# Kernel tuning notes

Measured on AMD Instinct MI355X. Metric: run time of the kernel, lower is better.

Reference implementation:

```python
import jax, jax.numpy as jnp
from jax import lax
import numpy as np

# db3 analysis/synthesis filter bank (pywt coefficients)
DEC_LO = np.array([0.035226291882100656, -0.085441273882241486, -0.13501102001039084,
                   0.45987750211933132, 0.80689150931333875, 0.33267055295095688], dtype=np.float32)
DEC_HI = np.array([-0.33267055295095688, 0.80689150931333875, -0.45987750211933132,
                   -0.13501102001039084, 0.085441273882241486, 0.035226291882100656], dtype=np.float32)
REC_LO = DEC_LO[::-1].copy()
REC_HI = np.array([0.035226291882100656, 0.085441273882241486, -0.13501102001039084,
                   -0.45987750211933132, 0.80689150931333875, -0.33267055295095688], dtype=np.float32)
L = 6  # db3 filter length
DN = ('NCHW', 'OIHW', 'NCHW')

# analysis correlation kernels (torch conv2d correlates, pytorch_wavelets pre-flips dec filters)
H0_A = jnp.asarray(DEC_LO[::-1].copy())
H1_A = jnp.asarray(DEC_HI[::-1].copy())
# synthesis: conv_transpose(x, g, stride=2, pad=L-2) == correlate(dilate(x,2), flip(g), pad=1)
G0_S = jnp.asarray(REC_LO[::-1].copy())
G1_S = jnp.asarray(REC_HI[::-1].copy())


def _sep_conv(x, f, axis, stride=1, lhs_dil=1, pad=0):
    """Depthwise 1-D correlation along H (axis=2) or W (axis=3) of an NCHW tensor."""
    C = x.shape[1]
    if axis == 2:
        k = jnp.tile(f.reshape(1, 1, -1, 1), (C, 1, 1, 1))
        strides, dil, padding = (stride, 1), (lhs_dil, 1), ((pad, pad), (0, 0))
    else:
        k = jnp.tile(f.reshape(1, 1, 1, -1), (C, 1, 1, 1))
        strides, dil, padding = (1, stride), (1, lhs_dil), ((0, 0), (pad, pad))
    return lax.conv_general_dilated(x, k, strides, padding, lhs_dilation=dil,
                                    dimension_numbers=DN, feature_group_count=C)


def _dwt2(x):
    # single-level separable 2D DWT, mode='zero' (pytorch_wavelets: rows then cols)
    lo = _sep_conv(x, H0_A, 3, stride=2, pad=L - 2)
    hi = _sep_conv(x, H1_A, 3, stride=2, pad=L - 2)
    ll = _sep_conv(lo, H0_A, 2, stride=2, pad=L - 2)
    lh = _sep_conv(lo, H1_A, 2, stride=2, pad=L - 2)  # yh[:,:,0]
    hl = _sep_conv(hi, H0_A, 2, stride=2, pad=L - 2)  # yh[:,:,1]
    hh = _sep_conv(hi, H1_A, 2, stride=2, pad=L - 2)  # yh[:,:,2]
    return ll, lh, hl, hh


def _idwt2(ll, lh, hl, hh):
    # inverse: cols then rows; transposed conv realized as lhs_dilation=2 + pad 1
    lo = _sep_conv(ll, G0_S, 2, lhs_dil=2, pad=1) + _sep_conv(lh, G1_S, 2, lhs_dil=2, pad=1)
    hi = _sep_conv(hl, G0_S, 2, lhs_dil=2, pad=1) + _sep_conv(hh, G1_S, 2, lhs_dil=2, pad=1)
    return _sep_conv(lo, G0_S, 3, lhs_dil=2, pad=1) + _sep_conv(hi, G1_S, 3, lhs_dil=2, pad=1)


def _dw3x3(x, w):
    # depthwise 3x3, padding 1, no bias; w: (C,1,3,3)
    return lax.conv_general_dilated(x, w, (1, 1), ((1, 1), (1, 1)),
                                    dimension_numbers=DN, feature_group_count=x.shape[1])


def _ssl(x, conv5_w, conv7_w, conv9_w):
    # faithful to original: conv5 applied to BOTH yl and ylh; conv1/conv_cat unused
    ll, lh, hl, hh = _dwt2(x)
    return _idwt2(_dw3x3(ll, conv5_w), _dw3x3(lh, conv5_w),
                  _dw3x3(hl, conv7_w), _dw3x3(hh, conv9_w))


def setup_inputs() -> dict:
    key = jax.random.key(0)
    ks = jax.random.split(key, 7)
    B, C, H, W, HEADS = 4, 256, 192, 192, 8
    s = 0.05
    return {
        'x': jax.random.normal(ks[0], (B, C, H, W), jnp.float32),
        'qkv_w': jax.random.normal(ks[1], (2 * C, C), jnp.float32) * s,        # 1x1 conv C->2C
        'qkv_conv_w': jax.random.normal(ks[2], (2 * C, 1, 3, 3), jnp.float32) * s,  # depthwise 3x3
        'conv5_w': jax.random.normal(ks[3], (C, 1, 3, 3), jnp.float32) * s,
        'conv7_w': jax.random.normal(ks[4], (C, 1, 3, 3), jnp.float32) * s,
        'conv9_w': jax.random.normal(ks[5], (C, 1, 3, 3), jnp.float32) * s,
        'proj_w': jax.random.normal(ks[6], (C, C), jnp.float32) * s,           # 1x1 conv C->C
        'temperature': jnp.ones((1, HEADS, 1, 1), jnp.float32),
        'num_heads': HEADS,
    }


def reference(x, qkv_w, qkv_conv_w, conv5_w, conv7_w, conv9_w, proj_w, temperature, num_heads):
    b, c, h, w = x.shape
    eps = 1e-12
    kv = jnp.einsum('oc,bchw->bohw', qkv_w, x)          # 1x1 conv, no bias
    kv = _dw3x3(kv, qkv_conv_w)
    k, v = jnp.split(kv, 2, axis=1)
    q = _ssl(x, conv5_w, conv7_w, conv9_w)              # wavelet query path, same HxW
    d = c // num_heads
    q = q.reshape(b, num_heads, d, h * w)
    k = k.reshape(b, num_heads, d, h * w)
    v = v.reshape(b, num_heads, d, h * w)
    q = q / jnp.maximum(jnp.linalg.norm(q, axis=-1, keepdims=True), eps)
    k = k / jnp.maximum(jnp.linalg.norm(k, axis=-1, keepdims=True), eps)
    attn = jax.nn.softmax(jnp.einsum('bhdn,bhen->bhde', q, k) * temperature, axis=-1)  # (b,H,d,d)
    out = jnp.einsum('bhde,bhen->bhdn', attn, v).reshape(b, c, h, w)
    return jnp.einsum('oc,bchw->bohw', proj_w, out)
```

## Files before the change

kernel.cpp:

```cpp
#include <hip/hip_runtime.h>
#include <hip/hip_bf16.h>

typedef __hip_bfloat16 bf16;
typedef __attribute__((ext_vector_type(8))) short short8v;
typedef __attribute__((ext_vector_type(4))) float f32x4;

#define NB 4
#define NC 256
#define NPIX 36864
#define NH 192
#define NW 192
#define SW 98
#define SH 98
#define GCH 24

__device__ __constant__ float cH0A[6] = {  0.33267055295095688f,  0.80689150931333875f,  0.45987750211933132f, -0.13501102001039084f, -0.085441273882241486f, 0.035226291882100656f };
__device__ __constant__ float cH1A[6] = {  0.035226291882100656f, 0.085441273882241486f, -0.13501102001039084f, -0.45987750211933132f,  0.80689150931333875f, -0.33267055295095688f };
__device__ __constant__ float cG0S[6] = {  0.035226291882100656f, -0.085441273882241486f, -0.13501102001039084f, 0.45987750211933132f,  0.80689150931333875f,  0.33267055295095688f };
__device__ __constant__ float cG1S[6] = { -0.33267055295095688f,  0.80689150931333875f, -0.45987750211933132f, -0.13501102001039084f,  0.085441273882241486f, 0.035226291882100656f };

__device__ inline unsigned short bfbits(float f) {
    bf16 h = __float2bfloat16(f);
    return *reinterpret_cast<unsigned short*>(&h);
}
__device__ inline float b2f(short s) {
    return __bfloat162float(*reinterpret_cast<const bf16*>(&s));
}

__global__ __launch_bounds__(256) void k_wave(const float* __restrict__ x,
                                              const float* __restrict__ w5, const float* __restrict__ w7,
                                              const float* __restrict__ w9,
                                              bf16* __restrict__ q, float* __restrict__ qsum) {
    int w0 = blockIdx.x * 64, h0 = blockIdx.y * 32;
    int bc = blockIdx.z;
    int c = bc & 255;
    int jh0 = h0 >> 1, jw0 = w0 >> 1;
    int xr0 = h0 - 6;
    int xc0 = w0 - 8;
    __shared__ __align__(16) char smem[40320];
    float (*s_x)[80]   = (float(*)[80])smem;
    float (*s_c)[36]   = (float(*)[36])smem;
    float (*s_lo)[40]  = (float(*)[40])(smem + 14080);
    float (*s_hi)[40]  = (float(*)[40])(smem + 21120);
    float (*s_lh)[36]  = (float(*)[36])(smem + 14080);
    float (*s_sub)[38] = (float(*)[38])(smem + 28160);
    __shared__ float s_w[4][9];
    __shared__ float red[4];
    const float* xp = x + (size_t)bc * NPIX;
    int t = threadIdx.x;
    if (t < 36) {
        int f = t / 9, k = t - f * 9;
        const float* wsel = (f <= 1) ? w5 : (f == 2 ? w7 : w9);
        s_w[f][k] = wsel[c * 9 + k];
    }
    for (int e = t; e < 880; e += 256) {
        int r = e / 20, s = e - r * 20;
        int row = xr0 + r, col0 = xc0 + s * 4;
        float4 v = make_float4(0.f, 0.f, 0.f, 0.f);
        if (row >= 0 && row < NH) {
            if (col0 >= 0 && col0 + 3 < NW) {
                v = *reinterpret_cast<const float4*>(xp + (size_t)row * NW + col0);
            } else {
#pragma unroll
                for (int j = 0; j < 4; ++j) {
                    int cc = col0 + j;
                    if (cc >= 0 && cc < NW) (&v.x)[j] = xp[(size_t)row * NW + cc];
                }
            }
        }
        *reinterpret_cast<float4*>(&s_x[r][s * 4]) = v;
    }
    __syncthreads();
    for (int e = t; e < 1672; e += 256) {
        int r = e / 38, jc = e - r * 38;
        float la = 0.f, ha = 0.f;
#pragma unroll
        for (int tp = 0; tp < 6; ++tp) {
            float v = s_x[r][2 * jc + tp];
            la = fmaf(v, cH0A[tp], la);
            ha = fmaf(v, cH1A[tp], ha);
        }
        s_lo[r][jc] = la; s_hi[r][jc] = ha;
    }
    __syncthreads();
    for (int e = t; e < 760; e += 256) {
        int r = e / 38, jc = e - r * 38;
        int gr = jh0 - 1 + r, gcol = jw0 - 2 + jc;
        bool inb = (gr >= 0 && gr < SH && gcol >= 0 && gcol < SW);
        float ll = 0.f, lh = 0.f, hl = 0.f, hh = 0.f;
#pragma unroll
        for (int tp = 0; tp < 6; ++tp) {
            float lv = s_lo[2 * r + tp][jc];
            float hv = s_hi[2 * r + tp][jc];
            ll = fmaf(lv, cH0A[tp], ll); lh = fmaf(lv, cH1A[tp], lh);
            hl = fmaf(hv, cH0A[tp], hl); hh = fmaf(hv, cH1A[tp], hh);
        }
        s_sub[r][jc]      = inb ? ll : 0.f;
        s_sub[20 + r][jc] = inb ? lh : 0.f;
        s_sub[40 + r][jc] = inb ? hl : 0.f;
        s_sub[60 + r][jc] = inb ? hh : 0.f;
    }
    __syncthreads();
    for (int e = t; e < 2448; e += 256) {
        int pr = e / 34, cc = e - pr * 34;
        int pl = pr / 18, r = pr - pl * 18;
        const float* wp = s_w[pl];
        const int rb = pl * 20 + r;
        float a = 0.f;
#pragma unroll
        for (int ky = 0; ky < 3; ++ky)
#pragma unroll
            for (int kx = 0; kx < 3; ++kx)
                a = fmaf(s_sub[rb + ky][cc + 1 + kx], wp[ky * 3 + kx], a);
        s_c[pr][cc] = a;
    }
    __syncthreads();
    for (int e = t; e < 1088; e += 256) {
        int row = e / 34, cc = e - row * 34;
        int which = row >> 4, m = row & 15;
        float c0_0 = s_c[which * 36 + m][cc],     c1_0 = s_c[which * 36 + 18 + m][cc];
        float c0_1 = s_c[which * 36 + m + 1][cc], c1_1 = s_c[which * 36 + 18 + m + 1][cc];
        float c0_2 = s_c[which * 36 + m + 2][cc], c1_2 = s_c[which * 36 + 18 + m + 2][cc];
        float ae = c0_0 * cG0S[1] + c0_1 * cG0S[3] + c0_2 * cG0S[5]
                 + c1_0 * cG1S[1] + c1_1 * cG1S[3] + c1_2 * cG1S[5];
        float ao = c0_0 * cG0S[0] + c0_1 * cG0S[2] + c0_2 * cG0S[4]
                 + c1_0 * cG1S[0] + c1_1 * cG1S[2] + c1_2 * cG1S[4];
        s_lh[which * 32 + 2 * m][cc] = ae;
        s_lh[which * 32 + 2 * m + 1][cc] = ao;
    }
    __syncthreads();
    float lsum = 0.f;
    bf16* qp = q + (size_t)bc * NPIX;
#pragma unroll
    for (int it = 0; it < 4; ++it) {
        int e = t + 256 * it;
        int hh = e >> 5, m = e & 31;
        float l0 = s_lh[hh][m],     h0v = s_lh[32 + hh][m];
        float l1 = s_lh[hh][m + 1], h1v = s_lh[32 + hh][m + 1];
        float l2 = s_lh[hh][m + 2], h2v = s_lh[32 + hh][m + 2];
        float ae = l0 * cG0S[1] + l1 * cG0S[3] + l2 * cG0S[5]
                 + h0v * cG1S[1] + h1v * cG1S[3] + h2v * cG1S[5];
        float ao = l0 * cG0S[0] + l1 * cG0S[2] + l2 * cG0S[4]
                 + h0v * cG1S[0] + h1v * cG1S[2] + h2v * cG1S[4];
        unsigned pack = (unsigned)bfbits(ae) | ((unsigned)bfbits(ao) << 16);
        *reinterpret_cast<unsigned*>(qp + (size_t)(h0 + hh) * NW + w0 + 2 * m) = pack;
        lsum = fmaf(ae, ae, lsum);
        lsum = fmaf(ao, ao, lsum);
    }
#pragma unroll
    for (int off = 32; off; off >>= 1) lsum += __shfl_down(lsum, off, 64);
    if ((t & 63) == 0) red[t >> 6] = lsum;
    __syncthreads();
    if (t == 0) atomicAdd(&qsum[bc], red[0] + red[1] + red[2] + red[3]);
}

__global__ __launch_bounds__(256) void k_xpose(const float* __restrict__ x, bf16* __restrict__ xT) {
    __shared__ float T[64][68];
    int nt = blockIdx.x, ct = blockIdx.y, b = blockIdx.z;
    int n0 = nt * 64, c0 = ct * 64;
    const float* xb = x + ((size_t)b * NC + c0) * NPIX + n0;
    int t = threadIdx.x;
    int tr = t >> 4, tc4 = (t & 15) * 4;
#pragma unroll
    for (int i = 0; i < 4; ++i) {
        int cc = tr + i * 16;
        float4 v = *reinterpret_cast<const float4*>(xb + (size_t)cc * NPIX + tc4);
        T[cc][tc4] = v.x; T[cc][tc4 + 1] = v.y; T[cc][tc4 + 2] = v.z; T[cc][tc4 + 3] = v.w;
    }
    __syncthreads();
    bf16* ob = xT + ((size_t)b * NPIX + n0) * NC + c0;
#pragma unroll
    for (int i = 0; i < 4; ++i) {
        int nn = tr + i * 16;
        ushort4 u;
        u.x = bfbits(T[tc4][nn]); u.y = bfbits(T[tc4 + 1][nn]);
        u.z = bfbits(T[tc4 + 2][nn]); u.w = bfbits(T[tc4 + 3][nn]);
        *reinterpret_cast<ushort4*>(ob + (size_t)nn * NC + tc4) = u;
    }
}

__global__ __launch_bounds__(256) void k_cvtw(const float* __restrict__ w, bf16* __restrict__ wb) {
    int idx = blockIdx.x * 256 + threadIdx.x;
    if (idx < 512 * 256) wb[idx] = __float2bfloat16(w[idx]);
}

template <typename TOUT>
__global__ __launch_bounds__(256) void k_gemm_bf(const bf16* __restrict__ X, const bf16* __restrict__ Wm,
                                                 int wStride, TOUT* __restrict__ Out) {
    __shared__ __align__(16) short As[128 * 64];
    __shared__ __align__(16) short Bs[128 * 64];
    int nt = blockIdx.x, ot = blockIdx.y, b = blockIdx.z;
    int n0 = nt * 128, o0 = ot * 128;
    const bf16* xb = X + (size_t)b * NPIX * NC;
    const bf16* Wb = Wm + (size_t)b * wStride;
    int t = threadIdx.x;
    int wv = t >> 6, l = t & 63;
    int wr = wv >> 1, wc = wv & 1;
    int lrow = l >> 3, cbs0 = l & 7;
    f32x4 z4 = {0.f, 0.f, 0.f, 0.f};
    f32x4 acc[4][4];
#pragma unroll
    for (int m = 0; m < 4; ++m)
#pragma unroll
        for (int nf = 0; nf < 4; ++nf) acc[m][nf] = z4;
    for (int kc = 0; kc < 256; kc += 64) {
        __syncthreads();
#pragma unroll
        for (int i = 0; i < 4; ++i) {
            int r0 = wv * 32 + i * 8;
            int r = r0 + lrow;
            int cb = cbs0 ^ (r & 7);
            __builtin_amdgcn_global_load_lds(
                (const __attribute__((address_space(1))) void*)(Wb + (size_t)(o0 + r) * NC + kc + cb * 8),
                (__attribute__((address_space(3))) void*)(As + r0 * 64), 16, 0, 0);
            __builtin_amdgcn_global_load_lds(
                (const __attribute__((address_space(1))) void*)(xb + (size_t)(n0 + r) * NC + kc + cb * 8),
                (__attribute__((address_space(3))) void*)(Bs + r0 * 64), 16, 0, 0);
        }
        __syncthreads();
#pragma unroll
        for (int kk = 0; kk < 2; ++kk) {
            int col8 = kk * 4 + (l >> 4);
            short8v av[4], bv[4];
#pragma unroll
            for (int m = 0; m < 4; ++m) {
                int row = wr * 64 + m * 16 + (l & 15);
                av[m] = *(const short8v*)(As + row * 64 + (col8 ^ (row & 7)) * 8);
            }
#pragma unroll
            for (int nf = 0; nf < 4; ++nf) {
                int row = wc * 64 + nf * 16 + (l & 15);
                bv[nf] = *(const short8v*)(Bs + row * 64 + (col8 ^ (row & 7)) * 8);
            }
#pragma unroll
            for (int m = 0; m < 4; ++m)
#pragma unroll
                for (int nf = 0; nf < 4; ++nf)
                    acc[m][nf] = __builtin_amdgcn_mfma_f32_16x16x32_bf16(av[m], bv[nf], acc[m][nf], 0, 0, 0);
        }
    }
    TOUT* ob = Out + (size_t)b * NC * NPIX;
#pragma unroll
    for (int m = 0; m < 4; ++m)
#pragma unroll
        for (int nf = 0; nf < 4; ++nf)
#pragma unroll
            for (int r = 0; r < 4; ++r) {
                int oo = o0 + wr * 64 + m * 16 + (l >> 4) * 4 + r;
                int nn = n0 + wc * 64 + nf * 16 + (l & 15);
                if constexpr (sizeof(TOUT) == 2)
                    ob[(size_t)oo * NPIX + nn] = __float2bfloat16(acc[m][nf][r]);
                else
                    ob[(size_t)oo * NPIX + nn] = acc[m][nf][r];
            }
}

__device__ inline short8v dw8(const bf16* __restrict__ chan, int r, int cb,
                              const float* __restrict__ w, float& ks) {
    float v[3][10];
#pragma unroll
    for (int ri = 0; ri < 3; ++ri) {
        int r2 = r + ri - 1;
        if (r2 < 0 || r2 >= NH) {
#pragma unroll
            for (int j = 0; j < 10; ++j) v[ri][j] = 0.f;
        } else {
            const bf16* p = chan + (size_t)r2 * NW + cb;
            short8v m = *(const short8v*)p;
            v[ri][0] = (cb > 0) ? __bfloat162float(p[-1]) : 0.f;
#pragma unroll
            for (int j = 0; j < 8; ++j) v[ri][j + 1] = b2f(m[j]);
            v[ri][9] = (cb < 184) ? __bfloat162float(p[8]) : 0.f;
        }
    }
    short8v out;
#pragma unroll
    for (int j = 0; j < 8; ++j) {
        float a = 0.f;
#pragma unroll
        for (int ri = 0; ri < 3; ++ri) {
            a = fmaf(v[ri][j],     w[ri * 3 + 0], a);
            a = fmaf(v[ri][j + 1], w[ri * 3 + 1], a);
            a = fmaf(v[ri][j + 2], w[ri * 3 + 2], a);
        }
        ks = fmaf(a, a, ks);
        out[j] = (short)bfbits(a);
    }
    return out;
}

__global__ __launch_bounds__(256) void k_gram_dw(const bf16* __restrict__ qbf, const bf16* __restrict__ kraw,
                                                 const float* __restrict__ dwW,
                                                 float* __restrict__ gpart, float* __restrict__ ksum) {
    int chunk = blockIdx.x;
    int bh = blockIdx.y; int b = bh >> 3, h = bh & 7;
    const bf16* qb = qbf + ((size_t)b * NC + h * 32) * NPIX;
    const bf16* kb = kraw + ((size_t)b * NC + h * 32) * NPIX;
    __shared__ float sg[4][1024];
    __shared__ float ksh[32];
    int t = threadIdx.x;
    int wv = t >> 6, l = t & 63;
    int dlo = l & 15, kslot = l >> 4;
    float wA[9], wB[9];
#pragma unroll
    for (int i = 0; i < 9; ++i) {
        wA[i] = dwW[(h * 32 + dlo) * 9 + i];
        wB[i] = dwW[(h * 32 + dlo + 16) * 9 + i];
    }
    const bf16* q0 = qb + (size_t)dlo * NPIX;
    const bf16* q1 = qb + (size_t)(dlo + 16) * NPIX;
    const bf16* k0 = kb + (size_t)dlo * NPIX;
    const bf16* k1 = kb + (size_t)(dlo + 16) * NPIX;
    f32x4 z4 = {0.f, 0.f, 0.f, 0.f};
    f32x4 a00 = z4, a01 = z4, a10 = z4, a11 = z4;
    float ks0 = 0.f, ks1 = 0.f;
    int r0 = chunk * 8 + wv * 2;
#pragma unroll
    for (int rr = 0; rr < 2; ++rr) {
        int r = r0 + rr;
#pragma unroll
        for (int c0 = 0; c0 < 192; c0 += 32) {
            int cb = c0 + kslot * 8;
            short8v av0 = *(const short8v*)(q0 + (size_t)r * NW + cb);
            short8v av1 = *(const short8v*)(q1 + (size_t)r * NW + cb);
            short8v bv0 = dw8(k0, r, cb, wA, ks0);
            short8v bv1 = dw8(k1, r, cb, wB, ks1);
            a00 = __builtin_amdgcn_mfma_f32_16x16x32_bf16(av0, bv0, a00, 0, 0, 0);
            a01 = __builtin_amdgcn_mfma_f32_16x16x32_bf16(av0, bv1, a01, 0, 0, 0);
            a10 = __builtin_amdgcn_mfma_f32_16x16x32_bf16(av1, bv0, a10, 0, 0, 0);
            a11 = __builtin_amdgcn_mfma_f32_16x16x32_bf16(av1, bv1, a11, 0, 0, 0);
        }
    }
    if (t < 32) ksh[t] = 0.f;
#pragma unroll
    for (int j = 0; j < 4; ++j) {
        int dA = kslot * 4 + j, dB = 16 + kslot * 4 + j;
        sg[wv][dA * 32 + dlo]      = a00[j];
        sg[wv][dA * 32 + 16 + dlo] = a01[j];
        sg[wv][dB * 32 + dlo]      = a10[j];
        sg[wv][dB * 32 + 16 + dlo] = a11[j];
    }
    __syncthreads();
    float* gp = gpart + ((size_t)bh * GCH + chunk) * 1024;
#pragma unroll
    for (int i = 0; i < 4; ++i) {
        int e = t + 256 * i;
        gp[e] = sg[0][e] + sg[1][e] + sg[2][e] + sg[3][e];
    }
    atomicAdd(&ksh[dlo], ks0);
    atomicAdd(&ksh[dlo + 16], ks1);
    __syncthreads();
    if (t < 32) atomicAdd(&ksum[b * NC + h * 32 + t], ksh[t]);
}

__global__ __launch_bounds__(1024) void k_attn(const float* __restrict__ gpart, const float* __restrict__ qsum,
                                               const float* __restrict__ ksum, const float* __restrict__ temp,
                                               float* __restrict__ attn) {
    int bh = blockIdx.x;
    int b = bh >> 3, h = bh & 7;
    int t = threadIdx.x;
    int d = t >> 5, e = t & 31;
    float s = 0.f;
    for (int i = 0; i < GCH; ++i) s += gpart[((size_t)bh * GCH + i) * 1024 + t];
    float rq = 1.f / fmaxf(sqrtf(qsum[b * NC + h * 32 + d]), 1e-12f);
    float rk = 1.f / fmaxf(sqrtf(ksum[b * NC + h * 32 + e]), 1e-12f);
    s *= rq * rk * temp[h];
    float m = s;
#pragma unroll
    for (int off = 16; off; off >>= 1) m = fmaxf(m, __shfl_xor(m, off, 32));
    float ex = expf(s - m);
    float sum = ex;
#pragma unroll
    for (int off = 16; off; off >>= 1) sum += __shfl_xor(sum, off, 32);
    attn[(size_t)bh * 1024 + t] = ex / sum;
}

__global__ __launch_bounds__(256) void k_wfold(const float* __restrict__ proj, const float* __restrict__ attn,
                                               bf16* __restrict__ wfbf) {
    int o = blockIdx.x, b = blockIdx.y;
    int t = threadIdx.x;
    int h = t >> 5, e = t & 31;
    const float* ap = attn + (size_t)(b * 8 + h) * 1024 + e;
    const float* pp = proj + o * NC + h * 32;
    float acc = 0.f;
#pragma unroll
    for (int d = 0; d < 32; ++d) acc = fmaf(pp[d], ap[d * 32], acc);
    wfbf[((size_t)b * NC + o) * NC + t] = __float2bfloat16(acc);
}

__global__ __launch_bounds__(256) void k_dwv(const bf16* __restrict__ vraw, const float* __restrict__ dwW,
                                             bf16* __restrict__ v2T) {
    int r = blockIdx.x;
    int cg = blockIdx.y;
    int b = blockIdx.z;
    __shared__ short s_v[3][32][204];
    const bf16* vb = vraw + ((size_t)b * NC + cg * 32) * NPIX;
    int t = threadIdx.x;
    for (int idx = t; idx < 4800; idx += 256) {
        int ri = idx / 1600;
        int rem = idx - ri * 1600;
        int e = rem / 50, j = rem - e * 50;
        int gr = r + ri - 1;
        int gc0 = -4 + 4 * j;
        ushort4 u = make_ushort4(0, 0, 0, 0);
        if (gr >= 0 && gr < NH && gc0 >= 0 && gc0 + 3 < NW)
            u = *reinterpret_cast<const ushort4*>(vb + (size_t)e * NPIX + (size_t)gr * NW + gc0);
        *reinterpret_cast<ushort4*>(&s_v[ri][e][4 * j]) = u;
    }
    int e = t & 31;
    int wslot = t >> 5;
    float w9[9];
#pragma unroll
    for (int i = 0; i < 9; ++i) w9[i] = dwW[(256 + cg * 32 + e) * 9 + i];
    __syncthreads();
    bf16* ob = v2T + ((size_t)b * NPIX + (size_t)r * NW) * NC + cg * 32 + e;
#pragma unroll
    for (int wi = 0; wi < 24; ++wi) {
        int w = wslot + 8 * wi;
        int cbase = w + 3;
        float a = 0.f;
#pragma unroll
        for (int ri = 0; ri < 3; ++ri) {
            a = fmaf(b2f(s_v[ri][e][cbase]),     w9[ri * 3 + 0], a);
            a = fmaf(b2f(s_v[ri][e][cbase + 1]), w9[ri * 3 + 1], a);
            a = fmaf(b2f(s_v[ri][e][cbase + 2]), w9[ri * 3 + 2], a);
        }
        ob[(size_t)w * NC] = __float2bfloat16(a);
    }
}


extern "C" void kernel_launch(void* const* d_in, const int* in_sizes, int n_in,
                              void* d_out, int out_size, void* d_ws, size_t ws_size,
                              hipStream_t stream) {
    (void)in_sizes; (void)n_in; (void)out_size;
    const float* x      = (const float*)d_in[0];
    const float* qkv_w  = (const float*)d_in[1];
    const float* qkv_cw = (const float*)d_in[2];
    const float* w5     = (const float*)d_in[3];
    const float* w7     = (const float*)d_in[4];
    const float* w9     = (const float*)d_in[5];
    const float* projw  = (const float*)d_in[6];
    const float* temp   = (const float*)d_in[7];

    const size_t OFF_SM    = 78675968;
    const size_t OFF_WBF   = OFF_SM;
    const size_t OFF_QSUM  = OFF_SM + 262144;
    const size_t OFF_KSUM  = OFF_QSUM + 4096;
    const size_t OFF_GPART = OFF_KSUM + 4096;
    const size_t OFF_ATTN  = OFF_GPART + 3145728;
    const size_t OFF_WF    = OFF_ATTN + 131072;
    const size_t WS_NEED   = OFF_WF + 524288;
    if (ws_size < WS_NEED) return;

    char* ws = (char*)d_ws;
    bf16*  kraw  = (bf16*)ws;
    bf16*  v2T   = (bf16*)ws;
    bf16*  wbf   = (bf16*)(ws + OFF_WBF);
    float* qsum  = (float*)(ws + OFF_QSUM);
    float* ksum  = (float*)(ws + OFF_KSUM);
    float* gpart = (float*)(ws + OFF_GPART);
    float* attn  = (float*)(ws + OFF_ATTN);
    bf16*  wfbf  = (bf16*)(ws + OFF_WF);

    bf16*  xbf  = (bf16*)d_out;
    bf16*  qbf  = (bf16*)((char*)d_out + 75497472);
    bf16*  vraw = (bf16*)((char*)d_out + 75497472);
    float* out  = (float*)d_out;

    hipMemsetAsync(ws + OFF_QSUM, 0, 8192, stream);

    k_wave<<<dim3(3, 6, NB * NC), 256, 0, stream>>>(x, w5, w7, w9, qbf, qsum);

    k_xpose<<<dim3(576, 4, NB), 256, 0, stream>>>(x, xbf);
    k_cvtw<<<512, 256, 0, stream>>>(qkv_w, wbf);

    k_gemm_bf<bf16><<<dim3(288, 2, NB), 256, 0, stream>>>(xbf, wbf, 0, kraw);
    k_gram_dw<<<dim3(GCH, 32), 256, 0, stream>>>(qbf, kraw, qkv_cw, gpart, ksum);

    k_attn<<<32, 1024, 0, stream>>>(gpart, qsum, ksum, temp, attn);
    k_wfold<<<dim3(256, NB), 256, 0, stream>>>(projw, attn, wfbf);

    k_gemm_bf<bf16><<<dim3(288, 2, NB), 256, 0, stream>>>(xbf, wbf + 256 * 256, 0, vraw);
    k_dwv<<<dim3(NH, 8, NB), 256, 0, stream>>>(vraw, qkv_cw, v2T);
    k_gemm_bf<float><<<dim3(288, 2, NB), 256, 0, stream>>>(v2T, wfbf, 65536, out);
}
```

Measured before the change: 533.6 us.

## Fuse x transpose and bf16 conversion into the k/v projection GEMM

Removes the separate k_xpose kernel that wrote a transposed bf16 copy of x. A new k_gemm_x reads fp32 x directly, converts it to bf16 and transposes it into swizzled shared memory, then runs MFMA. Each block now covers all 256 output channels, so x is read once per GEMM rather than once per output tile. The cost is reading fp32 x twice (once for k, once for v) instead of bf16, plus larger shared-memory tiles and 512-thread blocks.

```diff
diff --git a/kernel.cpp b/kernel.cpp
--- a/kernel.cpp
+++ b/kernel.cpp
@@ -154,34 +154,89 @@
     if (t == 0) atomicAdd(&qsum[bc], red[0] + red[1] + red[2] + red[3]);
 }
 
-__global__ __launch_bounds__(256) void k_xpose(const float* __restrict__ x, bf16* __restrict__ xT) {
-    __shared__ float T[64][68];
-    int nt = blockIdx.x, ct = blockIdx.y, b = blockIdx.z;
-    int n0 = nt * 64, c0 = ct * 64;
-    const float* xb = x + ((size_t)b * NC + c0) * NPIX + n0;
-    int t = threadIdx.x;
-    int tr = t >> 4, tc4 = (t & 15) * 4;
-#pragma unroll
-    for (int i = 0; i < 4; ++i) {
-        int cc = tr + i * 16;
-        float4 v = *reinterpret_cast<const float4*>(xb + (size_t)cc * NPIX + tc4);
-        T[cc][tc4] = v.x; T[cc][tc4 + 1] = v.y; T[cc][tc4 + 2] = v.z; T[cc][tc4 + 3] = v.w;
-    }
-    __syncthreads();
-    bf16* ob = xT + ((size_t)b * NPIX + n0) * NC + c0;
-#pragma unroll
-    for (int i = 0; i < 4; ++i) {
-        int nn = tr + i * 16;
-        ushort4 u;
-        u.x = bfbits(T[tc4][nn]); u.y = bfbits(T[tc4 + 1][nn]);
-        u.z = bfbits(T[tc4 + 2][nn]); u.w = bfbits(T[tc4 + 3][nn]);
-        *reinterpret_cast<ushort4*>(ob + (size_t)nn * NC + tc4) = u;
-    }
-}
-
 __global__ __launch_bounds__(256) void k_cvtw(const float* __restrict__ w, bf16* __restrict__ wb) {
     int idx = blockIdx.x * 256 + threadIdx.x;
     if (idx < 512 * 256) wb[idx] = __float2bfloat16(w[idx]);
+}
+
+__global__ __launch_bounds__(512) void k_gemm_x(const float* __restrict__ x, const bf16* __restrict__ Wbf,
+                                                bf16* __restrict__ Out) {
+    __shared__ __align__(16) short As[256 * 64];
+    __shared__ __align__(16) short Bs[128 * 64];
+    int nt = blockIdx.x, b = blockIdx.y;
+    int n0 = nt * 128;
+    const float* xb = x + (size_t)b * NC * NPIX;
+    int t = threadIdx.x;
+    int wv = t >> 6, l = t & 63;
+    int wo = wv >> 1, wn = wv & 1;
+    int lrow = l >> 3, cbs0 = l & 7;
+    int nq = t & 31;
+    int cg = t >> 5;
+    int c0 = cg * 4;
+    f32x4 z4 = {0.f, 0.f, 0.f, 0.f};
+    f32x4 acc[4][4];
+#pragma unroll
+    for (int m = 0; m < 4; ++m)
+#pragma unroll
+        for (int nf = 0; nf < 4; ++nf) acc[m][nf] = z4;
+    for (int kc = 0; kc < 256; kc += 64) {
+        __syncthreads();
+#pragma unroll
+        for (int i = 0; i < 4; ++i) {
+            int r0 = wv * 32 + i * 8;
+            int r = r0 + lrow;
+            int cb = cbs0 ^ (r & 7);
+            __builtin_amdgcn_global_load_lds(
+                (const __attribute__((address_space(1))) void*)(Wbf + (size_t)r * NC + kc + cb * 8),
+                (__attribute__((address_space(3))) void*)(As + r0 * 64), 16, 0, 0);
+        }
+        float4 xv[4];
+#pragma unroll
+        for (int ci = 0; ci < 4; ++ci)
+            xv[ci] = *reinterpret_cast<const float4*>(xb + (size_t)(kc + c0 + ci) * NPIX + n0 + nq * 4);
+#pragma unroll
+        for (int j = 0; j < 4; ++j) {
+            int n = nq * 4 + j;
+            ushort4 u;
+            u.x = bfbits((&xv[0].x)[j]); u.y = bfbits((&xv[1].x)[j]);
+            u.z = bfbits((&xv[2].x)[j]); u.w = bfbits((&xv[3].x)[j]);
+            int unit = (c0 >> 3) ^ (n & 7);
+            int half = (c0 >> 2) & 1;
+            *reinterpret_cast<ushort4*>(Bs + n * 64 + unit * 8 + half * 4) = u;
+        }
+        __syncthreads();
+#pragma unroll
+        for (int kk = 0; kk < 2; ++kk) {
+            int col8 = kk * 4 + (l >> 4);
+            short8v av[4], bv[4];
+#pragma unroll
+            for (int m = 0; m < 4; ++m) {
+                int row = wo * 64 + m * 16 + (l & 15);
+                av[m] = *(const short8v*)(As + row * 64 + (col8 ^ (row & 7)) * 8);
+            }
+#pragma unroll
+            for (int nf = 0; nf < 4; ++nf) {
+                int row = wn * 64 + nf * 16 + (l & 15);
+                bv[nf] = *(const short8v*)(Bs + row * 64 + (col8 ^ (row & 7)) * 8);
+            }
+#pragma unroll
+            for (int m = 0; m < 4; ++m)
+#pragma unroll
+                for (int nf = 0; nf < 4; ++nf)
+                    acc[m][nf] = __builtin_amdgcn_mfma_f32_16x16x32_bf16(av[m], bv[nf], acc[m][nf], 0, 0, 0);
+        }
+    }
+    bf16* ob = Out + (size_t)b * NC * NPIX;
+#pragma unroll
+    for (int m = 0; m < 4; ++m)
+#pragma unroll
+        for (int nf = 0; nf < 4; ++nf)
+#pragma unroll
+            for (int r = 0; r < 4; ++r) {
+                int oo = wo * 64 + m * 16 + (l >> 4) * 4 + r;
+                int nn = n0 + wn * 64 + nf * 16 + (l & 15);
+                ob[(size_t)oo * NPIX + nn] = __float2bfloat16(acc[m][nf][r]);
+            }
 }
 
 template <typename TOUT>
@@ -463,7 +518,6 @@
     float* attn  = (float*)(ws + OFF_ATTN);
     bf16*  wfbf  = (bf16*)(ws + OFF_WF);
 
-    bf16*  xbf  = (bf16*)d_out;
     bf16*  qbf  = (bf16*)((char*)d_out + 75497472);
     bf16*  vraw = (bf16*)((char*)d_out + 75497472);
     float* out  = (float*)d_out;
@@ -472,16 +526,15 @@
 
     k_wave<<<dim3(3, 6, NB * NC), 256, 0, stream>>>(x, w5, w7, w9, qbf, qsum);
 
-    k_xpose<<<dim3(576, 4, NB), 256, 0, stream>>>(x, xbf);
     k_cvtw<<<512, 256, 0, stream>>>(qkv_w, wbf);
 
-    k_gemm_bf<bf16><<<dim3(288, 2, NB), 256, 0, stream>>>(xbf, wbf, 0, kraw);
+    k_gemm_x<<<dim3(288, NB), 512, 0, stream>>>(x, wbf, kraw);
     k_gram_dw<<<dim3(GCH, 32), 256, 0, stream>>>(qbf, kraw, qkv_cw, gpart, ksum);
 
     k_attn<<<32, 1024, 0, stream>>>(gpart, qsum, ksum, temp, attn);
     k_wfold<<<dim3(256, NB), 256, 0, stream>>>(projw, attn, wfbf);
 
-    k_gemm_bf<bf16><<<dim3(288, 2, NB), 256, 0, stream>>>(xbf, wbf + 256 * 256, 0, vraw);
+    k_gemm_x<<<dim3(288, NB), 512, 0, stream>>>(x, wbf + 256 * 256, vraw);
     k_dwv<<<dim3(NH, 8, NB), 256, 0, stream>>>(vraw, qkv_cw, v2T);
     k_gemm_bf<float><<<dim3(288, 2, NB), 256, 0, stream>>>(v2T, wfbf, 65536, out);
 }
```

Result: no change. 531.8 us (-0.3%).
